# Kernel tuning notes

Hardware: AMD Instinct MI355X
Metric: run time of the kernel (lower is better)

The kernel has to match this reference:

```python
import jax, jax.numpy as jnp
import numpy as np

# ---- Projective geometric algebra G(3,0,1): 16-dim multivectors -------------
_METRIC = (0.0, 1.0, 1.0, 1.0)  # e0^2 = 0 (projective), e1..e3^2 = 1
_MASKS = sorted(range(16), key=lambda m: (bin(m).count('1'), m))  # blades by (grade, mask)
_IDX = {m: i for i, m in enumerate(_MASKS)}


def _blade_mul(a, b):
    swaps = sum(bin(a >> (i + 1)).count('1') for i in range(4) if (b >> i) & 1)
    coef = -1.0 if swaps % 2 else 1.0
    common = a & b
    for i in range(4):
        if (common >> i) & 1:
            coef *= _METRIC[i]
    return a ^ b, coef


_Cnp = np.zeros((16, 16, 16), dtype=np.float32)
for _i, _a in enumerate(_MASKS):
    for _j, _b in enumerate(_MASKS):
        _m, _c = _blade_mul(_a, _b)
        if _c != 0.0:
            _Cnp[_i, _j, _IDX[_m]] = _c
C = jnp.asarray(_Cnp)                                   # geometric-product structure tensor
GRADE = np.array([bin(m).count('1') for m in _MASKS])   # grade of each blade (static)
INNER = jnp.asarray(np.array([0.0 if (m & 1) else 1.0 for m in _MASKS], dtype=np.float32))  # invariant inner product drops e0 blades
_T_IDX = np.array([_IDX[3], _IDX[5], _IDX[9]])          # e01,e02,e03: translation slots


def equi_linear(x, w):
    # x: [b,n,in,16], w: [5,out,in] -- one channel-mixing matrix per grade (Pin-equivariant)
    Wc = w[GRADE]  # [16,out,in]
    return jnp.einsum('bnic,coi->bnoc', x, Wc)


def equi_layernorm(x, eps=1e-6):
    ip = jnp.sum(x * x * INNER, axis=-1)  # [b,n,ch] invariant squared norms
    denom = jnp.sqrt(jnp.mean(ip, axis=-1, keepdims=True) / 16.0 + eps)
    return x / denom[..., None]


def geometric_product(l, r):
    # l,r: [b,n,h,16] -> channel-wise geometric product
    return jnp.einsum('bnhi,bnhj,ijk->bnhk', l, r, C)


def attention(x, wq, wk, wv, wo):
    q, k, v = equi_linear(x, wq), equi_linear(x, wk), equi_linear(x, wv)
    scale = 1.0 / np.sqrt(16.0 * q.shape[-2])
    logits = jnp.einsum('bnhc,bmhc,c->bnm', q, k, INNER) * scale  # invariant inner product
    attn = jax.nn.softmax(logits, axis=-1)
    out = jnp.einsum('bnm,bmhc->bnhc', attn, v)
    return equi_linear(out, wo)


def mlp(x, w1, w2):
    h = equi_linear(x, w1)          # [b,n,2H,16]
    l, r = jnp.split(h, 2, axis=-2)
    gp = geometric_product(l, r)    # geometric bilinear
    z = gp * jax.nn.gelu(gp[..., 0:1])  # gated GELU on scalar component
    return equi_linear(z, w2)


def gatr_forward(mv, w_in, w_out, wq, wk, wv, wo, w_mlp1, w_mlp2):
    h = equi_linear(mv, w_in)
    for blk in range(wq.shape[0]):  # fixed small number of blocks
        h = h + attention(equi_layernorm(h), wq[blk], wk[blk], wv[blk], wo[blk])
        h = h + mlp(equi_layernorm(h), w_mlp1[blk], w_mlp2[blk])
    return equi_linear(h, w_out)


INV, VM = 32, 1  # input_inv_dimension, input_vector_multiplicity (== output sizes)


def setup_inputs() -> dict:
    key = jax.random.key(0)
    ks = jax.random.split(key, 9)
    B, N, H, BLK = 4, 4096, 5, 3

    def w(k, shape, fan_in):
        return jax.random.normal(k, shape, jnp.float32) / np.sqrt(fan_in)

    return {
        'x': jax.random.normal(ks[0], (B, N, INV + 3 * VM), jnp.float32),
        'w_in': w(ks[1], (5, H, INV), INV),
        'w_out': w(ks[2], (5, INV, H), H),
        'wq': w(ks[3], (BLK, 5, H, H), H),
        'wk': w(ks[4], (BLK, 5, H, H), H),
        'wv': w(ks[5], (BLK, 5, H, H), H),
        'wo': w(ks[6], (BLK, 5, H, H), H),
        'w_mlp1': w(ks[7], (BLK, 5, 2 * H, H), H),
        'w_mlp2': w(ks[8], (BLK, 5, H, H), H),
    }


def reference(x, w_in, w_out, wq, wk, wv, wo, w_mlp1, w_mlp2):
    b, n, _ = x.shape
    inv = x[..., :INV]                       # [b,n,32] invariants
    vec = x[..., INV:].reshape(b, n, VM, 3)  # [b,n,1,3] vectors
    mv = jnp.zeros((b, n, INV, 16), x.dtype)
    mv = mv.at[..., 0].set(inv)              # embed_scalar into scalar slot
    vec_mv = jnp.zeros((b, n, VM, 16), x.dtype)
    vec_mv = vec_mv.at[..., 0].set(1.0)      # translation versor identity part
    vec_mv = vec_mv.at[..., _T_IDX].set(vec) # e0i slots
    mv = mv.at[..., :VM, :].set(vec_mv)      # overwrites first VM channels (as in torch source)
    out = gatr_forward(mv, w_in, w_out, wq, wk, wv, wo, w_mlp1, w_mlp2)
    s_out = out[..., :INV, 0]                              # [b,n,32]
    v_out = out[..., :VM, _T_IDX].reshape(b, n, VM * 3)    # [b,n,3]
    return jnp.concatenate([s_out, v_out], axis=-1)
```

## Files before the change

### kernel.cpp

```cpp
#include <hip/hip_runtime.h>
#include <hip/hip_bf16.h>
#include <math.h>

typedef __attribute__((ext_vector_type(8)))  _Float16 f16x8;
typedef __attribute__((ext_vector_type(2)))  __fp16   fp16v2;
typedef __attribute__((ext_vector_type(16))) float    f32x16;


namespace ga {
constexpr int MASKS[16] = {0,1,2,4,8,3,5,6,9,10,12,7,11,13,14,15};
constexpr int popc4(int x){ return (x&1)+((x>>1)&1)+((x>>2)&1)+((x>>3)&1); }
constexpr int idx_of(int m){ int r=-1; for(int i=0;i<16;i++) if(MASKS[i]==m) r=i; return r; }
struct GPTab {
  int cnt[16];
  signed char ii[16][16];
  signed char jj[16][16];
  float ss[16][16];
};
constexpr GPTab make_gptab(){
  GPTab t{};
  for(int i=0;i<16;i++) for(int j=0;j<16;j++){
    int a=MASKS[i], b=MASKS[j];
    if((a&b&1)!=0) continue;
    int sw=0;
    for(int bi=0;bi<4;bi++) if((b>>bi)&1) sw += popc4(a>>(bi+1));
    int k = idx_of(a^b);
    int c = t.cnt[k];
    t.ii[k][c]=(signed char)i; t.jj[k][c]=(signed char)j;
    t.ss[k][c]=(sw&1)? -1.0f : 1.0f;
    t.cnt[k]=c+1;
  }
  return t;
}
}

__device__ const ga::GPTab GPT = ga::make_gptab();
__constant__ int GRADE16[16] = {0,1,1,1,1,2,2,2,2,2,2,3,3,3,3,4};
__constant__ int CPOS16[16] = {0,-1,1,2,3,-1,-1,4,-1,5,6,-1,-1,-1,7,-1};

#define NTOK 16384
#define NSEQ 4096
#define NB 4
#define QP 64
#define VTROWS 80
#define THR2 11.54f

__global__ __launch_bounds__(256) void k_init_h(
    const float* __restrict__ x, const float* __restrict__ w_in,
    float* __restrict__ h)
{
  int gid = blockIdx.x*256 + threadIdx.x;
  if (gid >= NTOK*5) return;
  int o = gid % 5, token = gid / 5;
  const float* xt = x + (size_t)token*35;
  const float* w0 = w_in + o*32;
  float s = w0[0];
  #pragma unroll
  for (int i=1;i<32;i++) s += w0[i]*xt[i];
  float w2c = w_in[2*160 + o*32 + 0];
  float* ht = h + (size_t)token*80 + o*16;
  #pragma unroll
  for (int c=0;c<16;c++) ht[c] = 0.f;
  ht[0] = s;
  ht[5] = w2c*xt[32];
  ht[6] = w2c*xt[33];
  ht[8] = w2c*xt[34];
}

__global__ __launch_bounds__(256) void k_ln_qkv(
    const float* __restrict__ h,
    const float* __restrict__ wq, const float* __restrict__ wk,
    const float* __restrict__ wv,
    _Float16* __restrict__ qf, _Float16* __restrict__ kf,
    _Float16* __restrict__ vf)
{
  int tid = threadIdx.x;
  int c   = tid & 15;
  int token = blockIdx.x*16 + (tid>>4);
  int b = token >> 12;
  int n = token & 4095;
  int vt_tile = b*128 + (n>>5);
  int nn = n & 31;
  int t  = (nn>>2)&3;
  int t2 = ((t<<1)|(t>>1))&3;
  int vt_col = (nn&3) | (t2<<2) | (nn&16);
  const float* ht = h + (size_t)token*80;
  float hv[5];
  #pragma unroll
  for (int i=0;i<5;i++) hv[i] = ht[i*16 + c];
  bool inner = (0x469D >> c) & 1;
  float part = 0.f;
  if (inner) {
    #pragma unroll
    for (int i=0;i<5;i++) part += hv[i]*hv[i];
  }
  part += __shfl_xor(part, 1);
  part += __shfl_xor(part, 2);
  part += __shfl_xor(part, 4);
  part += __shfl_xor(part, 8);
  float denom = sqrtf(part*(1.f/80.f) + 1e-6f);
  float rinv = 1.f/denom;
  float rln[5];
  #pragma unroll
  for (int i=0;i<5;i++) rln[i] = hv[i]*rinv;

  int g = GRADE16[c];
  int cp = CPOS16[c];
  const float scaleq = 0.16129820906f;
  #pragma unroll
  for (int o=0;o<5;o++) {
    const float* wqr = wq + g*25 + o*5;
    const float* wkr = wk + g*25 + o*5;
    const float* wvr = wv + g*25 + o*5;
    float aq=0.f, ak=0.f, av=0.f;
    #pragma unroll
    for (int i=0;i<5;i++) {
      aq += rln[i]*wqr[i];
      ak += rln[i]*wkr[i];
      av += rln[i]*wvr[i];
    }
    vf[((size_t)vt_tile*VTROWS + o*16 + c)*32 + vt_col] = (_Float16)av;
    if (inner) {
      size_t qo = (size_t)token*QP + o*8 + cp;
      qf[qo] = (_Float16)(aq*scaleq);
      kf[qo] = (_Float16)ak;
    }
  }
  if (c < 8) {
    size_t po = (size_t)token*QP + 40 + c;
    qf[po] = (_Float16)0.f;
    kf[po] = (_Float16)0.f;
  }
}

__global__ __launch_bounds__(256, 2) void k_attn_lds(
    const _Float16* __restrict__ qf, const _Float16* __restrict__ kf,
    const _Float16* __restrict__ vf,
    float* __restrict__ wsO, float* __restrict__ wsM,
    float* __restrict__ wsL, int nsplit)
{
  __shared__ __align__(16) char sK[2][4096];
  __shared__ __align__(16) char sV[2][5120];
  __shared__ __align__(16) float sF[4][32];
  int tid = threadIdx.x;
  int w  = tid >> 6;
  int l  = tid & 63;
  int ln = l & 31;
  int hf = l >> 5;
  int bid = blockIdx.x;
  int xcd = bid & 7;
  int b   = xcd & 3;
  int rest = bid >> 3;
  int qlo  = rest & 15;
  int z    = rest >> 4;
  int qgroup = (xcd>>2)*16 + qlo;
  int qtile = qgroup*4 + w;
  int rowbase = b*NSEQ + qtile*32;
  int ntiles = (NSEQ/nsplit) >> 5;
  int kbeg = z*(NSEQ/nsplit);

  const _Float16* qp = qf + (size_t)(rowbase + ln)*QP + hf*8;
  f16x8 q0 = *(const f16x8*)(qp);
  f16x8 q1 = *(const f16x8*)(qp + 16);
  f16x8 q2 = *(const f16x8*)(qp + 32);

  f32x16 acc0, acc1, acc2;
  #pragma unroll
  for (int r=0;r<16;r++){ acc0[r]=0.f; acc1[r]=0.f; acc2[r]=0.f; }
  float m = -1e30f, lsum = 0.f;

  int rdK0 = ln*128 + (((0+hf)^(ln&7))<<4);
  int rdK1 = ln*128 + (((2+hf)^(ln&7))<<4);
  int rdK2 = ln*128 + (((4+hf)^(ln&7))<<4);
  int vr0 = ln, vr1 = 32+ln, vr2 = 64+(ln&15);
  int sw0 = (vr0>>1)&3, sw1 = (vr1>>1)&3, sw2 = (vr2>>1)&3;
  int rdV00 = vr0*64 + (((hf  )^sw0)<<4);
  int rdV01 = vr0*64 + (((hf+2)^sw0)<<4);
  int rdV10 = vr1*64 + (((hf  )^sw1)<<4);
  int rdV11 = vr1*64 + (((hf+2)^sw1)<<4);
  int rdV20 = vr2*64 + (((hf  )^sw2)<<4);
  int rdV21 = vr2*64 + (((hf+2)^sw2)<<4);

  const _Float16* kfb = kf + (size_t)b*NSEQ*QP;
  const _Float16* vfb = vf + (size_t)(b*128)*(VTROWS*32);

  {
    const float4* kT = (const float4*)(kfb + (size_t)kbeg*QP);
    const float4* vT = (const float4*)(vfb + (size_t)(kbeg>>5)*(VTROWS*32));
    #pragma unroll
    for (int i=w; i<9; i+=4) {
      float4 d = (i<4) ? kT[i*64 + l] : vT[(i-4)*64 + l];
      if (i<4) {
        int gid = i*64 + l;
        *(float4*)(sK[0] + ((gid>>3)*128 + (((gid&7)^((gid>>3)&7))<<4))) = d;
      } else {
        int gid = (i-4)*64 + l;
        *(float4*)(sV[0] + ((gid>>2)*64 + (((gid&3)^((gid>>3)&3))<<4))) = d;
      }
    }
  }
  __syncthreads();

  for (int t=0; t<ntiles; ++t) {
    int cur = t & 1;
    float4 stg0, stg1, stg2; int i2=-1;
    if (t+1 < ntiles) {
      int koffn = kbeg + (t+1)*32;
      const float4* kT = (const float4*)(kfb + (size_t)koffn*QP);
      const float4* vT = (const float4*)(vfb + (size_t)(koffn>>5)*(VTROWS*32));
      stg0 = kT[w*64+l];
      stg1 = vT[w*64+l];
      if (w==0) { i2 = 8; stg2 = vT[4*64+l]; }
    }

    f16x8 kc0 = *(const f16x8*)(sK[cur] + rdK0);
    f16x8 kc1 = *(const f16x8*)(sK[cur] + rdK1);
    f16x8 kc2 = *(const f16x8*)(sK[cur] + rdK2);

    f32x16 S;
    #pragma unroll
    for (int r=0;r<16;r++) S[r]=0.f;
    S = __builtin_amdgcn_mfma_f32_32x32x16_f16(kc0, q0, S, 0,0,0);
    S = __builtin_amdgcn_mfma_f32_32x32x16_f16(kc1, q1, S, 0,0,0);
    S = __builtin_amdgcn_mfma_f32_32x32x16_f16(kc2, q2, S, 0,0,0);

    float t01 = fmaxf(S[0],S[1]),   t23 = fmaxf(S[2],S[3]);
    float t45 = fmaxf(S[4],S[5]),   t67 = fmaxf(S[6],S[7]);
    float t89 = fmaxf(S[8],S[9]),   tab = fmaxf(S[10],S[11]);
    float tcd = fmaxf(S[12],S[13]), tef = fmaxf(S[14],S[15]);
    float u0 = fmaxf(t01,t23), u1 = fmaxf(t45,t67);
    float u2 = fmaxf(t89,tab), u3 = fmaxf(tcd,tef);
    float tmax = fmaxf(fmaxf(u0,u1), fmaxf(u2,u3));
    tmax = fmaxf(tmax, __shfl_xor(tmax, 32));
    if (!__all(tmax <= m + THR2)) {
      float mn = fmaxf(m, tmax);
      float f = exp2f(m - mn);
      lsum *= f;
      m = mn;
      if (hf==0) sF[w][ln] = f;
      float fv[16];
      *(float4*)&fv[0]  = *(const float4*)&sF[w][ 0 + hf*4];
      *(float4*)&fv[4]  = *(const float4*)&sF[w][ 8 + hf*4];
      *(float4*)&fv[8]  = *(const float4*)&sF[w][16 + hf*4];
      *(float4*)&fv[12] = *(const float4*)&sF[w][24 + hf*4];
      #pragma unroll
      for (int r=0;r<16;r++){ float fr=fv[r]; acc0[r]*=fr; acc1[r]*=fr; acc2[r]*=fr; }
    }
    float p[16];
    #pragma unroll
    for (int r=0;r<16;r++) p[r] = exp2f(S[r] - m);
    float s0 = (p[0]+p[1]) + (p[2]+p[3]);
    float s1 = (p[4]+p[5]) + (p[6]+p[7]);
    float s2 = (p[8]+p[9]) + (p[10]+p[11]);
    float s3 = (p[12]+p[13]) + (p[14]+p[15]);
    lsum += (s0+s1) + (s2+s3);

    union { unsigned u[4]; f16x8 v; } A0, A1;
    #pragma unroll
    for (int e=0;e<4;e++) {
      union { fp16v2 h2; unsigned u; } cv;
      cv.h2 = __builtin_amdgcn_cvt_pkrtz(p[2*e], p[2*e+1]);
      A0.u[e] = cv.u;
    }
    #pragma unroll
    for (int e=0;e<4;e++) {
      union { fp16v2 h2; unsigned u; } cv;
      cv.h2 = __builtin_amdgcn_cvt_pkrtz(p[8+2*e], p[9+2*e]);
      A1.u[e] = cv.u;
    }

    f16x8 vc00 = *(const f16x8*)(sV[cur] + rdV00);
    f16x8 vc01 = *(const f16x8*)(sV[cur] + rdV01);
    f16x8 vc10 = *(const f16x8*)(sV[cur] + rdV10);
    f16x8 vc11 = *(const f16x8*)(sV[cur] + rdV11);
    f16x8 vc20 = *(const f16x8*)(sV[cur] + rdV20);
    f16x8 vc21 = *(const f16x8*)(sV[cur] + rdV21);

    acc0 = __builtin_amdgcn_mfma_f32_32x32x16_f16(A0.v, vc00, acc0, 0,0,0);
    acc0 = __builtin_amdgcn_mfma_f32_32x32x16_f16(A1.v, vc01, acc0, 0,0,0);
    acc1 = __builtin_amdgcn_mfma_f32_32x32x16_f16(A0.v, vc10, acc1, 0,0,0);
    acc1 = __builtin_amdgcn_mfma_f32_32x32x16_f16(A1.v, vc11, acc1, 0,0,0);
    acc2 = __builtin_amdgcn_mfma_f32_32x32x16_f16(A0.v, vc20, acc2, 0,0,0);
    acc2 = __builtin_amdgcn_mfma_f32_32x32x16_f16(A1.v, vc21, acc2, 0,0,0);

    if (t+1 < ntiles) {
      int nxt = (t+1) & 1;
      {
        int gid = w*64 + l;
        *(float4*)(sK[nxt] + ((gid>>3)*128 + (((gid&7)^((gid>>3)&7))<<4))) = stg0;
      }
      {
        int gid = w*64 + l;
        *(float4*)(sV[nxt] + ((gid>>2)*64 + (((gid&3)^((gid>>3)&3))<<4))) = stg1;
      }
      if (i2 == 8) {
        int gid = 4*64 + l;
        *(float4*)(sV[nxt] + ((gid>>2)*64 + (((gid&3)^((gid>>3)&3))<<4))) = stg2;
      }
    }
    __syncthreads();
  }

  lsum += __shfl_xor(lsum, 32);

  int pidx = (b*128 + qtile)*nsplit + z;
  if (hf==0) {
    wsM[pidx*32 + ln] = m;
    wsL[pidx*32 + ln] = lsum;
  }
  float* po = wsO + (size_t)pidx*32*80;
  #pragma unroll
  for (int r=0;r<16;r++) {
    int row = (r&3) + 8*(r>>2) + 4*hf;
    po[row*80 + ln]      = acc0[r];
    po[row*80 + 32 + ln] = acc1[r];
    if (ln < 16) po[row*80 + 64 + ln] = acc2[r];
  }
}

__global__ __launch_bounds__(256) void k_merge_mlp(
    const float* __restrict__ wsO, const float* __restrict__ wsM,
    const float* __restrict__ wsL, const float* __restrict__ wo,
    const float* __restrict__ w1, const float* __restrict__ w2,
    float* __restrict__ h, int nsplit)
{
  __shared__ float sh1[16][10][16];
  int tid = threadIdx.x;
  int c   = tid & 15;
  int tl  = tid >> 4;
  int token = blockIdx.x*16 + tl;
  int qrow = token & 31;
  int qt   = token >> 5;
  int g = GRADE16[c];
  float* ht = h + (size_t)token*80;

  int base = qt*nsplit;
  float M = -1e30f;
  for (int s=0; s<nsplit; ++s) M = fmaxf(M, wsM[(base+s)*32 + qrow]);
  float wgt[8];
  float L = 0.f;
  for (int s=0; s<nsplit; ++s) {
    wgt[s] = exp2f(wsM[(base+s)*32 + qrow] - M);
    L += wgt[s]*wsL[(base+s)*32 + qrow];
  }
  float invL = 1.f/L;
  float att[5];
  #pragma unroll
  for (int i=0;i<5;i++) {
    float a = 0.f;
    for (int s=0; s<nsplit; ++s)
      a += wgt[s]*wsO[((size_t)(base+s)*32 + qrow)*80 + i*16 + c];
    att[i] = a*invL;
  }

  float hv[5];
  #pragma unroll
  for (int o=0;o<5;o++) {
    const float* wor = wo + g*25 + o*5;
    float a = 0.f;
    #pragma unroll
    for (int i=0;i<5;i++) a += att[i]*wor[i];
    hv[o] = ht[o*16 + c] + a;
  }

  bool inner = (0x469D >> c) & 1;
  float part = 0.f;
  if (inner) {
    #pragma unroll
    for (int i=0;i<5;i++) part += hv[i]*hv[i];
  }
  part += __shfl_xor(part, 1);
  part += __shfl_xor(part, 2);
  part += __shfl_xor(part, 4);
  part += __shfl_xor(part, 8);
  float denom = sqrtf(part*(1.f/80.f) + 1e-6f);
  float rinv = 1.f/denom;
  float rln[5];
  #pragma unroll
  for (int i=0;i<5;i++) rln[i] = hv[i]*rinv;

  #pragma unroll
  for (int o=0;o<10;o++) {
    const float* w1r = w1 + g*50 + o*5;
    float a=0.f;
    #pragma unroll
    for (int i=0;i<5;i++) a += rln[i]*w1r[i];
    sh1[tl][o][c] = a;
  }
  __syncthreads();
  float gpv[5];
  #pragma unroll
  for (int hh=0; hh<5; hh++) {
    float a = 0.f;
    int n = GPT.cnt[c];
    for (int e=0; e<n; ++e) {
      a += GPT.ss[c][e]*sh1[tl][hh][GPT.ii[c][e]]*sh1[tl][5+hh][GPT.jj[c][e]];
    }
    gpv[hh] = a;
  }
  int lbase = (tid & 63) & ~15;
  #pragma unroll
  for (int hh=0;hh<5;hh++) {
    float g0 = __shfl(gpv[hh], lbase);
    float u  = 0.7978845608028654f*(g0 + 0.044715f*g0*g0*g0);
    float gate = 0.5f*g0*(1.f + tanhf(u));
    gpv[hh] *= gate;
  }
  #pragma unroll
  for (int o=0;o<5;o++) {
    const float* w2r = w2 + g*25 + o*5;
    float a=0.f;
    #pragma unroll
    for (int i=0;i<5;i++) a += gpv[i]*w2r[i];
    ht[o*16+c] = hv[o] + a;
  }
}

__global__ __launch_bounds__(256) void k_out(
    const float* __restrict__ h, const float* __restrict__ w_out,
    float* __restrict__ out)
{
  int gid = blockIdx.x*256 + threadIdx.x;
  if (gid >= NTOK*35) return;
  int j = gid % 35, token = gid / 35;
  const float* ht = h + (size_t)token*80;
  float a = 0.f;
  if (j < 32) {
    const float* w = w_out + j*5;
    #pragma unroll
    for (int i=0;i<5;i++) a += ht[i*16 + 0]*w[i];
  } else {
    int c = (j==32)?5:((j==33)?6:8);
    const float* w = w_out + 2*160 + 0*5;
    #pragma unroll
    for (int i=0;i<5;i++) a += ht[i*16 + c]*w[i];
  }
  out[gid] = a;
}

extern "C" void kernel_launch(void* const* d_in, const int* in_sizes, int n_in,
                              void* d_out, int out_size, void* d_ws, size_t ws_size,
                              hipStream_t stream) {
  const float* x     = (const float*)d_in[0];
  const float* w_in  = (const float*)d_in[1];
  const float* w_out = (const float*)d_in[2];
  const float* wq    = (const float*)d_in[3];
  const float* wk    = (const float*)d_in[4];
  const float* wv    = (const float*)d_in[5];
  const float* wo    = (const float*)d_in[6];
  const float* w1    = (const float*)d_in[7];
  const float* w2    = (const float*)d_in[8];
  float* out = (float*)d_out;

  char* p = (char*)d_ws;
  float* h = (float*)p;              p += (size_t)NTOK*80*4;
  _Float16* qf = (_Float16*)p;       p += (size_t)NTOK*QP*2;
  _Float16* kf = (_Float16*)p;       p += (size_t)NTOK*QP*2;
  _Float16* vf = (_Float16*)p;       p += (size_t)NB*128*VTROWS*32*2;
  size_t fixed = (size_t)((char*)p - (char*)d_ws);
  int nsplit = 4;
  if (fixed + (size_t)512*4*32*(80+2)*4 > ws_size) nsplit = 2;
  float* wsO = (float*)p;            p += (size_t)512*nsplit*32*80*4;
  float* wsM = (float*)p;            p += (size_t)512*nsplit*32*4;
  float* wsL = (float*)p;

  k_init_h<<<(NTOK*5 + 255)/256, 256, 0, stream>>>(x, w_in, h);
  for (int blk=0; blk<3; ++blk) {
    k_ln_qkv<<<NTOK/16, 256, 0, stream>>>(h, wq+blk*125, wk+blk*125, wv+blk*125,
                                          qf, kf, vf);
    k_attn_lds<<<128*nsplit, 256, 0, stream>>>(qf, kf, vf, wsO, wsM, wsL, nsplit);
    k_merge_mlp<<<NTOK/16, 256, 0, stream>>>(wsO, wsM, wsL, wo+blk*125,
                                             w1+blk*250, w2+blk*125, h, nsplit);
  }
  k_out<<<(NTOK*35 + 255)/256, 256, 0, stream>>>(h, w_out, out);
}
```

Measured before the change: 231.4 us.

## Fuse LN+QKV projection into init and merge-MLP kernels

Folds the per-block layernorm and Q/K/V projection into the preceding kernel: the initial embedding kernel now also computes the first block's QKV, and the merge+MLP kernel of blocks 0 and 1 computes the next block's QKV straight from the updated residual held in registers. This removes three kernel launches and the re-read of h from global memory before each attention. The init kernel is also reorganised to use 16 lanes per token with shuffle reductions. The cost is more registers per thread in the fused kernels, which may lower occupancy.

Measured after the change: 219.7 us. 5.1% less time.

```diff
diff --git a/kernel.cpp b/kernel.cpp
--- a/kernel.cpp
+++ b/kernel.cpp
@@ -45,38 +45,13 @@
 #define VTROWS 80
 #define THR2 11.54f
 
-__global__ __launch_bounds__(256) void k_init_h(
-    const float* __restrict__ x, const float* __restrict__ w_in,
-    float* __restrict__ h)
-{
-  int gid = blockIdx.x*256 + threadIdx.x;
-  if (gid >= NTOK*5) return;
-  int o = gid % 5, token = gid / 5;
-  const float* xt = x + (size_t)token*35;
-  const float* w0 = w_in + o*32;
-  float s = w0[0];
-  #pragma unroll
-  for (int i=1;i<32;i++) s += w0[i]*xt[i];
-  float w2c = w_in[2*160 + o*32 + 0];
-  float* ht = h + (size_t)token*80 + o*16;
-  #pragma unroll
-  for (int c=0;c<16;c++) ht[c] = 0.f;
-  ht[0] = s;
-  ht[5] = w2c*xt[32];
-  ht[6] = w2c*xt[33];
-  ht[8] = w2c*xt[34];
-}
-
-__global__ __launch_bounds__(256) void k_ln_qkv(
-    const float* __restrict__ h,
+__device__ __forceinline__ void ln_qkv_from_regs(
+    const float hv[5], int c, int token,
     const float* __restrict__ wq, const float* __restrict__ wk,
     const float* __restrict__ wv,
     _Float16* __restrict__ qf, _Float16* __restrict__ kf,
     _Float16* __restrict__ vf)
 {
-  int tid = threadIdx.x;
-  int c   = tid & 15;
-  int token = blockIdx.x*16 + (tid>>4);
   int b = token >> 12;
   int n = token & 4095;
   int vt_tile = b*128 + (n>>5);
@@ -84,10 +59,6 @@
   int t  = (nn>>2)&3;
   int t2 = ((t<<1)|(t>>1))&3;
   int vt_col = (nn&3) | (t2<<2) | (nn&16);
-  const float* ht = h + (size_t)token*80;
-  float hv[5];
-  #pragma unroll
-  for (int i=0;i<5;i++) hv[i] = ht[i*16 + c];
   bool inner = (0x469D >> c) & 1;
   float part = 0.f;
   if (inner) {
@@ -98,8 +69,7 @@
   part += __shfl_xor(part, 2);
   part += __shfl_xor(part, 4);
   part += __shfl_xor(part, 8);
-  float denom = sqrtf(part*(1.f/80.f) + 1e-6f);
-  float rinv = 1.f/denom;
+  float rinv = 1.f/sqrtf(part*(1.f/80.f) + 1e-6f);
   float rln[5];
   #pragma unroll
   for (int i=0;i<5;i++) rln[i] = hv[i]*rinv;
@@ -131,6 +101,47 @@
     qf[po] = (_Float16)0.f;
     kf[po] = (_Float16)0.f;
   }
+}
+
+__global__ __launch_bounds__(256) void k_init_qkv(
+    const float* __restrict__ x, const float* __restrict__ w_in,
+    const float* __restrict__ wq, const float* __restrict__ wk,
+    const float* __restrict__ wv,
+    float* __restrict__ h, _Float16* __restrict__ qf,
+    _Float16* __restrict__ kf, _Float16* __restrict__ vf)
+{
+  int tid = threadIdx.x;
+  int c   = tid & 15;
+  int token = blockIdx.x*16 + (tid>>4);
+  const float* xt = x + (size_t)token*35;
+  float* ht = h + (size_t)token*80;
+
+  float xa = (c==0) ? 1.f : xt[c];
+  float xb = xt[c+16];
+  float sv[5];
+  #pragma unroll
+  for (int o=0;o<5;o++) {
+    const float* w0 = w_in + o*32;
+    float partial = w0[c]*xa + w0[c+16]*xb;
+    partial += __shfl_xor(partial,1);
+    partial += __shfl_xor(partial,2);
+    partial += __shfl_xor(partial,4);
+    partial += __shfl_xor(partial,8);
+    sv[o] = partial;
+  }
+  float hv[5];
+  #pragma unroll
+  for (int o=0;o<5;o++) {
+    float w2c = w_in[2*160 + o*32];
+    float v = 0.f;
+    if (c==0) v = sv[o];
+    else if (c==5) v = w2c*xt[32];
+    else if (c==6) v = w2c*xt[33];
+    else if (c==8) v = w2c*xt[34];
+    hv[o] = v;
+    ht[o*16+c] = v;
+  }
+  ln_qkv_from_regs(hv, c, token, wq, wk, wv, qf, kf, vf);
 }
 
 __global__ __launch_bounds__(256, 2) void k_attn_lds(
@@ -318,14 +329,13 @@
   }
 }
 
-__global__ __launch_bounds__(256) void k_merge_mlp(
+__device__ __forceinline__ void merge_mlp_body(
     const float* __restrict__ wsO, const float* __restrict__ wsM,
     const float* __restrict__ wsL, const float* __restrict__ wo,
     const float* __restrict__ w1, const float* __restrict__ w2,
-    float* __restrict__ h, int nsplit)
-{
-  __shared__ float sh1[16][10][16];
-  int tid = threadIdx.x;
+    float* __restrict__ h, int nsplit,
+    float (*sh1)[10][16], int tid, float newh[5])
+{
   int c   = tid & 15;
   int tl  = tid >> 4;
   int token = blockIdx.x*16 + tl;
@@ -373,8 +383,7 @@
   part += __shfl_xor(part, 2);
   part += __shfl_xor(part, 4);
   part += __shfl_xor(part, 8);
-  float denom = sqrtf(part*(1.f/80.f) + 1e-6f);
-  float rinv = 1.f/denom;
+  float rinv = 1.f/sqrtf(part*(1.f/80.f) + 1e-6f);
   float rln[5];
   #pragma unroll
   for (int i=0;i<5;i++) rln[i] = hv[i]*rinv;
@@ -412,8 +421,39 @@
     float a=0.f;
     #pragma unroll
     for (int i=0;i<5;i++) a += gpv[i]*w2r[i];
-    ht[o*16+c] = hv[o] + a;
-  }
+    newh[o] = hv[o] + a;
+    ht[o*16+c] = newh[o];
+  }
+}
+
+__global__ __launch_bounds__(256) void k_merge_mlp_qkv(
+    const float* __restrict__ wsO, const float* __restrict__ wsM,
+    const float* __restrict__ wsL, const float* __restrict__ wo,
+    const float* __restrict__ w1, const float* __restrict__ w2,
+    const float* __restrict__ wqn, const float* __restrict__ wkn,
+    const float* __restrict__ wvn,
+    float* __restrict__ h, _Float16* __restrict__ qf,
+    _Float16* __restrict__ kf, _Float16* __restrict__ vf, int nsplit)
+{
+  __shared__ float sh1[16][10][16];
+  int tid = threadIdx.x;
+  float newh[5];
+  merge_mlp_body(wsO, wsM, wsL, wo, w1, w2, h, nsplit, sh1, tid, newh);
+  int c = tid & 15;
+  int token = blockIdx.x*16 + (tid>>4);
+  ln_qkv_from_regs(newh, c, token, wqn, wkn, wvn, qf, kf, vf);
+}
+
+__global__ __launch_bounds__(256) void k_merge_mlp(
+    const float* __restrict__ wsO, const float* __restrict__ wsM,
+    const float* __restrict__ wsL, const float* __restrict__ wo,
+    const float* __restrict__ w1, const float* __restrict__ w2,
+    float* __restrict__ h, int nsplit)
+{
+  __shared__ float sh1[16][10][16];
+  int tid = threadIdx.x;
+  float newh[5];
+  merge_mlp_body(wsO, wsM, wsL, wo, w1, w2, h, nsplit, sh1, tid, newh);
 }
 
 __global__ __launch_bounds__(256) void k_out(
@@ -464,13 +504,18 @@
   float* wsM = (float*)p;            p += (size_t)512*nsplit*32*4;
   float* wsL = (float*)p;
 
-  k_init_h<<<(NTOK*5 + 255)/256, 256, 0, stream>>>(x, w_in, h);
+  k_init_qkv<<<NTOK/16, 256, 0, stream>>>(x, w_in, wq, wk, wv, h, qf, kf, vf);
   for (int blk=0; blk<3; ++blk) {
-    k_ln_qkv<<<NTOK/16, 256, 0, stream>>>(h, wq+blk*125, wk+blk*125, wv+blk*125,
-                                          qf, kf, vf);
     k_attn_lds<<<128*nsplit, 256, 0, stream>>>(qf, kf, vf, wsO, wsM, wsL, nsplit);
-    k_merge_mlp<<<NTOK/16, 256, 0, stream>>>(wsO, wsM, wsL, wo+blk*125,
-                                             w1+blk*250, w2+blk*125, h, nsplit);
+    if (blk < 2) {
+      k_merge_mlp_qkv<<<NTOK/16, 256, 0, stream>>>(
+          wsO, wsM, wsL, wo+blk*125, w1+blk*250, w2+blk*125,
+          wq+(blk+1)*125, wk+(blk+1)*125, wv+(blk+1)*125,
+          h, qf, kf, vf, nsplit);
+    } else {
+      k_merge_mlp<<<NTOK/16, 256, 0, stream>>>(
+          wsO, wsM, wsL, wo+blk*125, w1+blk*250, w2+blk*125, h, nsplit);
+    }
   }
   k_out<<<(NTOK*35 + 255)/256, 256, 0, stream>>>(h, w_out, out);
 }
```
